# Kernel optimization log

Hardware: AMD Instinct MI355X
Metric: run time of the kernel (lower is better)

## Reference

```python
import jax, jax.numpy as jnp
import numpy as np

EMBED_DIM = 1024
NUM_HEADS = 16
HEAD_DIM = EMBED_DIM // NUM_HEADS
N, SEQ = 4, 2048


def setup_inputs() -> dict:
    key = jax.random.key(0)
    ks = jax.random.split(key, 9)
    s = 0.02
    return {
        "keys": jax.random.normal(ks[0], (N, SEQ, EMBED_DIM), jnp.float32),
        "values": jax.random.normal(ks[1], (N, SEQ, EMBED_DIM), jnp.float32),
        "queries": jax.random.normal(ks[2], (N, SEQ, EMBED_DIM), jnp.float32),
        "mask": jax.random.randint(ks[3], (N, 1, SEQ, SEQ), 0, 2, jnp.int32),
        "Wk": jax.random.normal(ks[4], (HEAD_DIM, HEAD_DIM), jnp.float32) * s,
        "Wv": jax.random.normal(ks[5], (HEAD_DIM, HEAD_DIM), jnp.float32) * s,
        "Wq": jax.random.normal(ks[6], (HEAD_DIM, HEAD_DIM), jnp.float32) * s,
        "Wo": jax.random.normal(ks[7], (EMBED_DIM, EMBED_DIM), jnp.float32) * s,
        "bo": jax.random.normal(ks[8], (EMBED_DIM,), jnp.float32) * s,
    }


def reference(keys, values, queries, mask, Wk, Wv, Wq, Wo, bo):
    n, key_len, _ = keys.shape
    value_len = values.shape[1]
    query_len = queries.shape[1]
    # Faithful to source: direct reshape (N, L, E) -> (N, H, L, D), no transpose.
    k = keys.reshape(n, NUM_HEADS, key_len, HEAD_DIM) @ Wk.T
    v = values.reshape(n, NUM_HEADS, value_len, HEAD_DIM) @ Wv.T
    q = queries.reshape(n, NUM_HEADS, query_len, HEAD_DIM) @ Wq.T
    # Scaled by sqrt(embed_dim) as in the original (not sqrt(head_dim)).
    energy = jnp.einsum('nhqd,nhkd->nhqk', q, k) / jnp.sqrt(jnp.float32(EMBED_DIM))
    energy = jnp.where(mask == 0, jnp.float32(-1e20), energy)
    attention = jax.nn.softmax(energy, axis=-1)
    att_out = jnp.einsum('nhql,nhld->nhqd', attention, v)
    att_out = att_out.reshape(n, query_len, NUM_HEADS * HEAD_DIM)
    return att_out @ Wo.T + bo
```

## Files before the change

kernel.cpp:

```cpp
#include <hip/hip_runtime.h>

#define SEQ 2048
#define HDIM 64
#define NH 16

typedef __bf16 bf16x8 __attribute__((ext_vector_type(8)));
typedef float f32x4 __attribute__((ext_vector_type(4)));
typedef unsigned short u16x8 __attribute__((ext_vector_type(8)));
typedef unsigned short u16x4 __attribute__((ext_vector_type(4)));
typedef _Float16 f16x4 __attribute__((ext_vector_type(4)));
typedef unsigned int u32x2 __attribute__((ext_vector_type(2)));
typedef unsigned long long u64;

__device__ __forceinline__ unsigned short f2bf(float f) {
  unsigned int u = __builtin_bit_cast(unsigned int, f);
  u = (u + 0x7FFFu + ((u >> 16) & 1u)) >> 16;
  return (unsigned short)u;
}

__device__ __forceinline__ bf16x8 cvt8(f32x4 a, f32x4 b) {
  u16x8 u;
  u[0] = f2bf(a[0]); u[1] = f2bf(a[1]); u[2] = f2bf(a[2]); u[3] = f2bf(a[3]);
  u[4] = f2bf(b[0]); u[5] = f2bf(b[1]); u[6] = f2bf(b[2]); u[7] = f2bf(b[3]);
  return __builtin_bit_cast(bf16x8, u);
}

__device__ __forceinline__ f32x4 mfma16(bf16x8 a, bf16x8 b, f32x4 c) {
  return __builtin_amdgcn_mfma_f32_16x16x32_bf16(a, b, c, 0, 0, 0);
}
__device__ __forceinline__ f32x4 mfma16h(f16x4 a, f16x4 b, f32x4 c) {
  return __builtin_amdgcn_mfma_f32_16x16x16f16(a, b, c, 0, 0, 0);
}

__device__ __forceinline__ f16x4 pk4h(float a, float b, float cc, float d) {
  auto h0 = __builtin_amdgcn_cvt_pkrtz(a, b);
  auto h1 = __builtin_amdgcn_cvt_pkrtz(cc, d);
  u32x2 u = { __builtin_bit_cast(unsigned int, h0),
              __builtin_bit_cast(unsigned int, h1) };
  return __builtin_bit_cast(f16x4, u);
}

#define QSCALE 0.045084220027780106f

__global__ __launch_bounds__(256) void qkv_proj(
    const float* __restrict__ keys, const float* __restrict__ values,
    const float* __restrict__ queries,
    const float* __restrict__ Wk, const float* __restrict__ Wv,
    const float* __restrict__ Wq,
    unsigned short* __restrict__ kb, unsigned short* __restrict__ vb,
    unsigned short* __restrict__ qb)
{
  const int which = blockIdx.y;
  const float* __restrict__ in = (which == 0) ? keys : (which == 1) ? values : queries;
  const float* __restrict__ W  = (which == 0) ? Wk   : (which == 1) ? Wv     : Wq;
  unsigned short* __restrict__ op = (which == 0) ? kb : (which == 1) ? vb : qb;
  const float osc = (which == 2) ? QSCALE : 1.0f;
  const bool asf16 = (which == 1);

  const int tid = threadIdx.x;
  const int w = tid >> 6, lane = tid & 63, c = lane & 15, quad = lane >> 4;

  bf16x8 bw[4][2];
  #pragma unroll
  for (int nt = 0; nt < 4; ++nt)
    #pragma unroll
    for (int hh = 0; hh < 2; ++hh) {
      const float* wr = W + (nt * 16 + c) * 64 + hh * 32 + quad * 8;
      bw[nt][hh] = cvt8(*(const f32x4*)wr, *(const f32x4*)(wr + 4));
    }

  const int m00 = blockIdx.x * 256 + w * 64;
  #pragma unroll
  for (int s = 0; s < 4; ++s) {
    const int m0 = m00 + s * 16;
    const float* xr = in + (size_t)(m0 + c) * 64;
    bf16x8 a0 = cvt8(*(const f32x4*)(xr + quad * 8), *(const f32x4*)(xr + quad * 8 + 4));
    bf16x8 a1 = cvt8(*(const f32x4*)(xr + 32 + quad * 8), *(const f32x4*)(xr + 36 + quad * 8));
    f32x4 acc[4] = {};
    #pragma unroll
    for (int nt = 0; nt < 4; ++nt) {
      acc[nt] = mfma16(a0, bw[nt][0], acc[nt]);
      acc[nt] = mfma16(a1, bw[nt][1], acc[nt]);
    }
    #pragma unroll
    for (int nt = 0; nt < 4; ++nt)
      #pragma unroll
      for (int r = 0; r < 4; ++r) {
        float v = acc[nt][r] * osc;
        unsigned short bits = asf16
            ? __builtin_bit_cast(unsigned short, (_Float16)v) : f2bf(v);
        op[(size_t)(m0 + quad * 4 + r) * 64 + nt * 16 + c] = bits;
      }
  }
}

__global__ __launch_bounds__(256) void cvt_wo(const float* __restrict__ src,
                                              unsigned short* __restrict__ dst)
{
  int i = (blockIdx.x * 256 + threadIdx.x) * 4;
  f32x4 v = *reinterpret_cast<const f32x4*>(src + i);
  u16x4 o;
  o[0] = f2bf(v[0]); o[1] = f2bf(v[1]); o[2] = f2bf(v[2]); o[3] = f2bf(v[3]);
  *reinterpret_cast<u16x4*>(dst + i) = o;
}

__global__ __launch_bounds__(256) void maskpack(const int* __restrict__ mask,
                                                u64* __restrict__ bits)
{
  const int wid = blockIdx.x * 4 + (threadIdx.x >> 6);
  const int lane = threadIdx.x & 63;
  const int* src = mask + (size_t)wid * 1024 + lane;
  u64* dst = bits + (size_t)wid * 16;
  #pragma unroll
  for (int i = 0; i < 16; ++i) {
    u64 b = __ballot(src[i * 64] != 0);
    if (lane == 0) dst[i] = b;
  }
}

__global__ __launch_bounds__(256, 4) void attn3(
    const unsigned short* __restrict__ qb, const unsigned short* __restrict__ kb,
    const unsigned short* __restrict__ vb, const u64* __restrict__ mbits,
    unsigned short* __restrict__ att)
{
  __shared__ __attribute__((aligned(16))) unsigned short Kl[64][72];
  __shared__ __attribute__((aligned(16))) unsigned short Vt[64][76];

  const int tid = threadIdx.x;
  const int w = tid >> 6, lane = tid & 63, c = lane & 15, quad = lane >> 4;
  const int h = blockIdx.y, n = blockIdx.z;
  const int q0 = blockIdx.x * 128;
  const size_t hb = (size_t)(n * NH + h) * (SEQ * HDIM);

  bf16x8 aq[2][2];
  #pragma unroll
  for (int qt = 0; qt < 2; ++qt) {
    const unsigned short* qr = qb + hb + (size_t)(q0 + qt * 64 + w * 16 + c) * HDIM;
    aq[qt][0] = *reinterpret_cast<const bf16x8*>(qr + quad * 8);
    aq[qt][1] = *reinterpret_cast<const bf16x8*>(qr + 32 + quad * 8);
  }

  f32x4 o[2][4] = {};
  f32x4 psv[2] = {};

  const u64* mb = mbits + ((size_t)n * SEQ + q0 + w * 16 + c) * 32;

  const int krow = tid >> 1, kcol = (tid & 1) * 32;
  const int vg = (tid >> 3) & 15, vd8 = tid & 7;

  for (int k0 = 0; k0 < SEQ; k0 += 64) {
    const int step = k0 >> 6;
    __syncthreads();
    if (tid < 128) {
      const unsigned short* s = kb + hb + (size_t)(k0 + krow) * HDIM + kcol;
      #pragma unroll
      for (int i = 0; i < 4; ++i)
        *(u16x8*)&Kl[krow][kcol + i * 8] = *(const u16x8*)(s + i * 8);
    } else {
      const unsigned short* s = vb + hb + (size_t)(k0 + vg * 4) * HDIM + vd8 * 8;
      u16x8 r0 = *(const u16x8*)(s);
      u16x8 r1 = *(const u16x8*)(s + HDIM);
      u16x8 r2 = *(const u16x8*)(s + 2 * HDIM);
      u16x8 r3 = *(const u16x8*)(s + 3 * HDIM);
      #pragma unroll
      for (int j = 0; j < 8; ++j) {
        u16x4 pk = { r0[j], r1[j], r2[j], r3[j] };
        *(u16x4*)&Vt[vd8 * 8 + j][vg * 4] = pk;
      }
    }
    __syncthreads();

    f32x4 e[2][4] = {};
    #pragma unroll
    for (int t = 0; t < 4; ++t) {
      bf16x8 kf0 = *reinterpret_cast<const bf16x8*>(&Kl[t * 16 + c][quad * 8]);
      bf16x8 kf1 = *reinterpret_cast<const bf16x8*>(&Kl[t * 16 + c][32 + quad * 8]);
      #pragma unroll
      for (int qt = 0; qt < 2; ++qt) {
        e[qt][t] = mfma16(kf0, aq[qt][0], e[qt][t]);
        e[qt][t] = mfma16(kf1, aq[qt][1], e[qt][t]);
      }
    }

    f16x4 pf[2][4];
    #pragma unroll
    for (int qt = 0; qt < 2; ++qt) {
      u64 bits = mb[(size_t)qt * 2048 + step] >> (quad * 4);
      unsigned int lo = (unsigned int)bits;
      unsigned int hi = (unsigned int)(bits >> 32);
      #pragma unroll
      for (int t = 0; t < 4; ++t) {
        unsigned int b = (t & 2) ? hi : lo;
        b >>= (t & 1) * 16;
        f32x4 ev = e[qt][t];
        float p0 = (b & 1u)        ? exp2f(ev[0]) : 0.0f;
        float p1 = ((b >> 1) & 1u) ? exp2f(ev[1]) : 0.0f;
        float p2 = ((b >> 2) & 1u) ? exp2f(ev[2]) : 0.0f;
        float p3 = ((b >> 3) & 1u) ? exp2f(ev[3]) : 0.0f;
        f32x4 pv = { p0, p1, p2, p3 };
        psv[qt] += pv;
        pf[qt][t] = pk4h(p0, p1, p2, p3);
      }
    }

    #pragma unroll
    for (int dt = 0; dt < 4; ++dt) {
      #pragma unroll
      for (int t = 0; t < 4; ++t) {
        f16x4 vf = __builtin_bit_cast(f16x4,
            *(const u16x4*)&Vt[dt * 16 + c][t * 16 + quad * 4]);
        o[0][dt] = mfma16h(vf, pf[0][t], o[0][dt]);
        o[1][dt] = mfma16h(vf, pf[1][t], o[1][dt]);
      }
    }
  }

  #pragma unroll
  for (int qt = 0; qt < 2; ++qt) {
    float s = (psv[qt][0] + psv[qt][1]) + (psv[qt][2] + psv[qt][3]);
    s += __shfl_xor(s, 16);
    s += __shfl_xor(s, 32);
    float inv = 1.0f / s;
    unsigned short* orow =
        att + hb + (size_t)(q0 + qt * 64 + w * 16 + c) * HDIM + quad * 4;
    #pragma unroll
    for (int dt = 0; dt < 4; ++dt) {
      u16x4 pk = { f2bf(o[qt][dt][0] * inv), f2bf(o[qt][dt][1] * inv),
                   f2bf(o[qt][dt][2] * inv), f2bf(o[qt][dt][3] * inv) };
      *(u16x4*)(orow + dt * 16) = pk;
    }
  }
}

__global__ __launch_bounds__(256) void out_proj2(
    const unsigned short* __restrict__ att, const unsigned short* __restrict__ wob,
    const float* __restrict__ bo, float* __restrict__ out)
{
  __shared__ __attribute__((aligned(16))) unsigned short As[128][72];
  __shared__ __attribute__((aligned(16))) unsigned short Bs[128][72];

  const int nb = blockIdx.x, mbk = blockIdx.y;
  const int tid = threadIdx.x;
  const int w = tid >> 6, lane = tid & 63, c = lane & 15, quad = lane >> 4;
  const int wm = w & 1, wn = w >> 1;
  const int m0 = mbk * 128, n0 = nb * 128;
  const int srow = tid >> 1, scol = (tid & 1) * 32;

  f32x4 acc[4][4] = {};

  for (int k0 = 0; k0 < 1024; k0 += 64) {
    __syncthreads();
    {
      const unsigned short* sa = att + (size_t)(m0 + srow) * 1024 + k0 + scol;
      const unsigned short* sb = wob + (size_t)(n0 + srow) * 1024 + k0 + scol;
      #pragma unroll
      for (int i = 0; i < 4; ++i)
        *(u16x8*)&As[srow][scol + i * 8] = *(const u16x8*)(sa + i * 8);
      #pragma unroll
      for (int i = 0; i < 4; ++i)
        *(u16x8*)&Bs[srow][scol + i * 8] = *(const u16x8*)(sb + i * 8);
    }
    __syncthreads();

    #pragma unroll
    for (int kk = 0; kk < 64; kk += 32) {
      bf16x8 af[4];
      #pragma unroll
      for (int mt = 0; mt < 4; ++mt)
        af[mt] = *reinterpret_cast<const bf16x8*>(&As[wm * 64 + mt * 16 + c][kk + quad * 8]);
      #pragma unroll
      for (int nt = 0; nt < 4; ++nt) {
        bf16x8 bf_ = *reinterpret_cast<const bf16x8*>(&Bs[wn * 64 + nt * 16 + c][kk + quad * 8]);
        #pragma unroll
        for (int mt = 0; mt < 4; ++mt)
          acc[mt][nt] = mfma16(af[mt], bf_, acc[mt][nt]);
      }
    }
  }

  #pragma unroll
  for (int nt = 0; nt < 4; ++nt) {
    const int col = n0 + wn * 64 + nt * 16 + c;
    const float bias = bo[col];
    #pragma unroll
    for (int mt = 0; mt < 4; ++mt)
      #pragma unroll
      for (int r = 0; r < 4; ++r)
        out[(size_t)(m0 + wm * 64 + mt * 16 + quad * 4 + r) * 1024 + col] =
            acc[mt][nt][r] + bias;
  }
}

extern "C" void kernel_launch(void* const* d_in, const int* in_sizes, int n_in,
                              void* d_out, int out_size, void* d_ws, size_t ws_size,
                              hipStream_t stream) {
  const float* keys    = (const float*)d_in[0];
  const float* values  = (const float*)d_in[1];
  const float* queries = (const float*)d_in[2];
  const int*   mask    = (const int*)d_in[3];
  const float* Wk      = (const float*)d_in[4];
  const float* Wv      = (const float*)d_in[5];
  const float* Wq      = (const float*)d_in[6];
  const float* Wo      = (const float*)d_in[7];
  const float* bo      = (const float*)d_in[8];
  float* out = (float*)d_out;

  const size_t T = (size_t)4 * NH * SEQ * HDIM;
  unsigned short* ws  = (unsigned short*)d_ws;
  unsigned short* kb  = ws;
  unsigned short* vb  = kb + T;
  unsigned short* qb  = vb + T;
  unsigned short* att = qb + T;
  unsigned short* wob = att + T;
  u64* mbits = (u64*)(wob + 1024 * 1024);

  qkv_proj<<<dim3(512, 3), 256, 0, stream>>>(keys, values, queries,
                                             Wk, Wv, Wq, kb, vb, qb);
  cvt_wo<<<dim3(1024), 256, 0, stream>>>(Wo, wob);
  maskpack<<<dim3(4096), 256, 0, stream>>>(mask, mbits);
  attn3<<<dim3(16, NH, 4), 256, 0, stream>>>(qb, kb, vb, mbits, att);
  out_proj2<<<dim3(8, 64), 256, 0, stream>>>(att, wob, bo, out);
}
```

Measured before the change: 377.8 us.

## Prefetch K/V tiles, mask via LUT, MFMA row sums, smaller out-proj tiles

Several changes land at once. The attention kernel now prefetches the next K/V tile into registers while the current one is processed, applies the mask by ANDing packed fp16 probabilities with a shared-memory lookup table, and computes softmax denominators with an extra MFMA against a ones vector instead of shuffles. qkv_proj swaps its MFMA operands so it can write packed 4-element stores. out_proj uses 64-row M tiles to double the block count. These add register pressure, and the fp16 row sums lose some precision.

```diff
diff --git a/kernel.cpp b/kernel.cpp
--- a/kernel.cpp
+++ b/kernel.cpp
@@ -60,13 +60,13 @@
   const int tid = threadIdx.x;
   const int w = tid >> 6, lane = tid & 63, c = lane & 15, quad = lane >> 4;
 
-  bf16x8 bw[4][2];
-  #pragma unroll
-  for (int nt = 0; nt < 4; ++nt)
+  bf16x8 aw[4][2];
+  #pragma unroll
+  for (int dt = 0; dt < 4; ++dt)
     #pragma unroll
     for (int hh = 0; hh < 2; ++hh) {
-      const float* wr = W + (nt * 16 + c) * 64 + hh * 32 + quad * 8;
-      bw[nt][hh] = cvt8(*(const f32x4*)wr, *(const f32x4*)(wr + 4));
+      const float* wr = W + (dt * 16 + c) * 64 + hh * 32 + quad * 8;
+      aw[dt][hh] = cvt8(*(const f32x4*)wr, *(const f32x4*)(wr + 4));
     }
 
   const int m00 = blockIdx.x * 256 + w * 64;
@@ -74,23 +74,27 @@
   for (int s = 0; s < 4; ++s) {
     const int m0 = m00 + s * 16;
     const float* xr = in + (size_t)(m0 + c) * 64;
-    bf16x8 a0 = cvt8(*(const f32x4*)(xr + quad * 8), *(const f32x4*)(xr + quad * 8 + 4));
-    bf16x8 a1 = cvt8(*(const f32x4*)(xr + 32 + quad * 8), *(const f32x4*)(xr + 36 + quad * 8));
+    bf16x8 x0 = cvt8(*(const f32x4*)(xr + quad * 8), *(const f32x4*)(xr + quad * 8 + 4));
+    bf16x8 x1 = cvt8(*(const f32x4*)(xr + 32 + quad * 8), *(const f32x4*)(xr + 36 + quad * 8));
     f32x4 acc[4] = {};
     #pragma unroll
-    for (int nt = 0; nt < 4; ++nt) {
-      acc[nt] = mfma16(a0, bw[nt][0], acc[nt]);
-      acc[nt] = mfma16(a1, bw[nt][1], acc[nt]);
-    }
-    #pragma unroll
-    for (int nt = 0; nt < 4; ++nt)
-      #pragma unroll
-      for (int r = 0; r < 4; ++r) {
-        float v = acc[nt][r] * osc;
-        unsigned short bits = asf16
-            ? __builtin_bit_cast(unsigned short, (_Float16)v) : f2bf(v);
-        op[(size_t)(m0 + quad * 4 + r) * 64 + nt * 16 + c] = bits;
-      }
+    for (int dt = 0; dt < 4; ++dt) {
+      acc[dt] = mfma16(aw[dt][0], x0, acc[dt]);
+      acc[dt] = mfma16(aw[dt][1], x1, acc[dt]);
+    }
+    unsigned short* orow = op + (size_t)(m0 + c) * 64 + quad * 4;
+    #pragma unroll
+    for (int dt = 0; dt < 4; ++dt) {
+      u16x4 pk;
+      if (asf16) {
+        pk = __builtin_bit_cast(u16x4,
+            pk4h(acc[dt][0], acc[dt][1], acc[dt][2], acc[dt][3]));
+      } else {
+        pk[0] = f2bf(acc[dt][0] * osc); pk[1] = f2bf(acc[dt][1] * osc);
+        pk[2] = f2bf(acc[dt][2] * osc); pk[3] = f2bf(acc[dt][3] * osc);
+      }
+      *(u16x4*)(orow + dt * 16) = pk;
+    }
   }
 }
 
@@ -118,13 +122,14 @@
   }
 }
 
-__global__ __launch_bounds__(256, 4) void attn3(
+__global__ __launch_bounds__(256, 4) void attn4(
     const unsigned short* __restrict__ qb, const unsigned short* __restrict__ kb,
     const unsigned short* __restrict__ vb, const u64* __restrict__ mbits,
     unsigned short* __restrict__ att)
 {
   __shared__ __attribute__((aligned(16))) unsigned short Kl[64][72];
   __shared__ __attribute__((aligned(16))) unsigned short Vt[64][76];
+  __shared__ unsigned int mlut[16][2];
 
   const int tid = threadIdx.x;
   const int w = tid >> 6, lane = tid & 63, c = lane & 15, quad = lane >> 4;
@@ -132,6 +137,12 @@
   const int q0 = blockIdx.x * 128;
   const size_t hb = (size_t)(n * NH + h) * (SEQ * HDIM);
 
+  if (tid < 16) {
+    unsigned m = tid;
+    mlut[m][0] = ((m & 1u) ? 0xFFFFu : 0u) | ((m & 2u) ? 0xFFFF0000u : 0u);
+    mlut[m][1] = ((m & 4u) ? 0xFFFFu : 0u) | ((m & 8u) ? 0xFFFF0000u : 0u);
+  }
+
   bf16x8 aq[2][2];
   #pragma unroll
   for (int qt = 0; qt < 2; ++qt) {
@@ -141,31 +152,57 @@
   }
 
   f32x4 o[2][4] = {};
-  f32x4 psv[2] = {};
+  f32x4 osum[2] = {};
+  const f16x4 ones = {(_Float16)1.f, (_Float16)1.f, (_Float16)1.f, (_Float16)1.f};
 
   const u64* mb = mbits + ((size_t)n * SEQ + q0 + w * 16 + c) * 32;
 
+  const bool isK = tid < 128;
   const int krow = tid >> 1, kcol = (tid & 1) * 32;
   const int vg = (tid >> 3) & 15, vd8 = tid & 7;
 
-  for (int k0 = 0; k0 < SEQ; k0 += 64) {
-    const int step = k0 >> 6;
+  const unsigned short* kptr = kb + hb + (size_t)krow * HDIM + kcol;
+  const unsigned short* vptr = vb + hb + (size_t)(vg * 4) * HDIM + vd8 * 8;
+
+  u16x8 st0, st1, st2, st3;
+  if (isK) {
+    st0 = *(const u16x8*)(kptr);
+    st1 = *(const u16x8*)(kptr + 8);
+    st2 = *(const u16x8*)(kptr + 16);
+    st3 = *(const u16x8*)(kptr + 24);
+  } else {
+    st0 = *(const u16x8*)(vptr);
+    st1 = *(const u16x8*)(vptr + HDIM);
+    st2 = *(const u16x8*)(vptr + 2 * HDIM);
+    st3 = *(const u16x8*)(vptr + 3 * HDIM);
+  }
+
+  for (int step = 0; step < 32; ++step) {
     __syncthreads();
-    if (tid < 128) {
-      const unsigned short* s = kb + hb + (size_t)(k0 + krow) * HDIM + kcol;
-      #pragma unroll
-      for (int i = 0; i < 4; ++i)
-        *(u16x8*)&Kl[krow][kcol + i * 8] = *(const u16x8*)(s + i * 8);
+    if (isK) {
+      *(u16x8*)&Kl[krow][kcol]      = st0;
+      *(u16x8*)&Kl[krow][kcol + 8]  = st1;
+      *(u16x8*)&Kl[krow][kcol + 16] = st2;
+      *(u16x8*)&Kl[krow][kcol + 24] = st3;
     } else {
-      const unsigned short* s = vb + hb + (size_t)(k0 + vg * 4) * HDIM + vd8 * 8;
-      u16x8 r0 = *(const u16x8*)(s);
-      u16x8 r1 = *(const u16x8*)(s + HDIM);
-      u16x8 r2 = *(const u16x8*)(s + 2 * HDIM);
-      u16x8 r3 = *(const u16x8*)(s + 3 * HDIM);
       #pragma unroll
       for (int j = 0; j < 8; ++j) {
-        u16x4 pk = { r0[j], r1[j], r2[j], r3[j] };
+        u16x4 pk = { st0[j], st1[j], st2[j], st3[j] };
         *(u16x4*)&Vt[vd8 * 8 + j][vg * 4] = pk;
+      }
+    }
+    if (step < 31) {
+      const size_t adv = (size_t)(step + 1) * 64 * HDIM;
+      if (isK) {
+        st0 = *(const u16x8*)(kptr + adv);
+        st1 = *(const u16x8*)(kptr + adv + 8);
+        st2 = *(const u16x8*)(kptr + adv + 16);
+        st3 = *(const u16x8*)(kptr + adv + 24);
+      } else {
+        st0 = *(const u16x8*)(vptr + adv);
+        st1 = *(const u16x8*)(vptr + adv + HDIM);
+        st2 = *(const u16x8*)(vptr + adv + 2 * HDIM);
+        st3 = *(const u16x8*)(vptr + adv + 3 * HDIM);
       }
     }
     __syncthreads();
@@ -182,24 +219,23 @@
       }
     }
 
+    u64 b0 = mb[step] >> (quad * 4);
+    u64 b1 = mb[2048 + step] >> (quad * 4);
+
     f16x4 pf[2][4];
     #pragma unroll
     for (int qt = 0; qt < 2; ++qt) {
-      u64 bits = mb[(size_t)qt * 2048 + step] >> (quad * 4);
-      unsigned int lo = (unsigned int)bits;
-      unsigned int hi = (unsigned int)(bits >> 32);
+      u64 bb = qt ? b1 : b0;
+      unsigned int lo = (unsigned int)bb, hi = (unsigned int)(bb >> 32);
       #pragma unroll
       for (int t = 0; t < 4; ++t) {
-        unsigned int b = (t & 2) ? hi : lo;
-        b >>= (t & 1) * 16;
+        unsigned int nib = (((t & 2) ? hi : lo) >> ((t & 1) * 16)) & 0xFu;
         f32x4 ev = e[qt][t];
-        float p0 = (b & 1u)        ? exp2f(ev[0]) : 0.0f;
-        float p1 = ((b >> 1) & 1u) ? exp2f(ev[1]) : 0.0f;
-        float p2 = ((b >> 2) & 1u) ? exp2f(ev[2]) : 0.0f;
-        float p3 = ((b >> 3) & 1u) ? exp2f(ev[3]) : 0.0f;
-        f32x4 pv = { p0, p1, p2, p3 };
-        psv[qt] += pv;
-        pf[qt][t] = pk4h(p0, p1, p2, p3);
+        f16x4 pk = pk4h(exp2f(ev[0]), exp2f(ev[1]), exp2f(ev[2]), exp2f(ev[3]));
+        u32x2 pw = __builtin_bit_cast(u32x2, pk);
+        pw[0] &= mlut[nib][0];
+        pw[1] &= mlut[nib][1];
+        pf[qt][t] = __builtin_bit_cast(f16x4, pw);
       }
     }
 
@@ -213,14 +249,16 @@
         o[1][dt] = mfma16h(vf, pf[1][t], o[1][dt]);
       }
     }
+    #pragma unroll
+    for (int t = 0; t < 4; ++t) {
+      osum[0] = mfma16h(ones, pf[0][t], osum[0]);
+      osum[1] = mfma16h(ones, pf[1][t], osum[1]);
+    }
   }
 
   #pragma unroll
   for (int qt = 0; qt < 2; ++qt) {
-    float s = (psv[qt][0] + psv[qt][1]) + (psv[qt][2] + psv[qt][3]);
-    s += __shfl_xor(s, 16);
-    s += __shfl_xor(s, 32);
-    float inv = 1.0f / s;
+    float inv = 1.0f / osum[qt][0];
     unsigned short* orow =
         att + hb + (size_t)(q0 + qt * 64 + w * 16 + c) * HDIM + quad * 4;
     #pragma unroll
@@ -232,47 +270,47 @@
   }
 }
 
-__global__ __launch_bounds__(256) void out_proj2(
+__global__ __launch_bounds__(256) void out_proj3(
     const unsigned short* __restrict__ att, const unsigned short* __restrict__ wob,
     const float* __restrict__ bo, float* __restrict__ out)
 {
-  __shared__ __attribute__((aligned(16))) unsigned short As[128][72];
+  __shared__ __attribute__((aligned(16))) unsigned short As[64][72];
   __shared__ __attribute__((aligned(16))) unsigned short Bs[128][72];
 
   const int nb = blockIdx.x, mbk = blockIdx.y;
   const int tid = threadIdx.x;
   const int w = tid >> 6, lane = tid & 63, c = lane & 15, quad = lane >> 4;
   const int wm = w & 1, wn = w >> 1;
-  const int m0 = mbk * 128, n0 = nb * 128;
-  const int srow = tid >> 1, scol = (tid & 1) * 32;
-
-  f32x4 acc[4][4] = {};
+  const int m0 = mbk * 64, n0 = nb * 128;
+  const int arow = tid >> 2, acol = (tid & 3) * 16;
+  const int brow = tid >> 1, bcol = (tid & 1) * 32;
+
+  f32x4 acc[2][4] = {};
 
   for (int k0 = 0; k0 < 1024; k0 += 64) {
     __syncthreads();
     {
-      const unsigned short* sa = att + (size_t)(m0 + srow) * 1024 + k0 + scol;
-      const unsigned short* sb = wob + (size_t)(n0 + srow) * 1024 + k0 + scol;
+      const unsigned short* sa = att + (size_t)(m0 + arow) * 1024 + k0 + acol;
+      const unsigned short* sb = wob + (size_t)(n0 + brow) * 1024 + k0 + bcol;
+      *(u16x8*)&As[arow][acol]     = *(const u16x8*)(sa);
+      *(u16x8*)&As[arow][acol + 8] = *(const u16x8*)(sa + 8);
       #pragma unroll
       for (int i = 0; i < 4; ++i)
-        *(u16x8*)&As[srow][scol + i * 8] = *(const u16x8*)(sa + i * 8);
-      #pragma unroll
-      for (int i = 0; i < 4; ++i)
-        *(u16x8*)&Bs[srow][scol + i * 8] = *(const u16x8*)(sb + i * 8);
+        *(u16x8*)&Bs[brow][bcol + i * 8] = *(const u16x8*)(sb + i * 8);
     }
     __syncthreads();
 
     #pragma unroll
     for (int kk = 0; kk < 64; kk += 32) {
-      bf16x8 af[4];
-      #pragma unroll
-      for (int mt = 0; mt < 4; ++mt)
-        af[mt] = *reinterpret_cast<const bf16x8*>(&As[wm * 64 + mt * 16 + c][kk + quad * 8]);
+      bf16x8 af[2];
+      #pragma unroll
+      for (int mt = 0; mt < 2; ++mt)
+        af[mt] = *reinterpret_cast<const bf16x8*>(&As[wm * 32 + mt * 16 + c][kk + quad * 8]);
       #pragma unroll
       for (int nt = 0; nt < 4; ++nt) {
         bf16x8 bf_ = *reinterpret_cast<const bf16x8*>(&Bs[wn * 64 + nt * 16 + c][kk + quad * 8]);
         #pragma unroll
-        for (int mt = 0; mt < 4; ++mt)
+        for (int mt = 0; mt < 2; ++mt)
           acc[mt][nt] = mfma16(af[mt], bf_, acc[mt][nt]);
       }
     }
@@ -283,10 +321,10 @@
     const int col = n0 + wn * 64 + nt * 16 + c;
     const float bias = bo[col];
     #pragma unroll
-    for (int mt = 0; mt < 4; ++mt)
+    for (int mt = 0; mt < 2; ++mt)
       #pragma unroll
       for (int r = 0; r < 4; ++r)
-        out[(size_t)(m0 + wm * 64 + mt * 16 + quad * 4 + r) * 1024 + col] =
+        out[(size_t)(m0 + wm * 32 + mt * 16 + quad * 4 + r) * 1024 + col] =
             acc[mt][nt][r] + bias;
   }
 }
@@ -318,6 +356,6 @@
                                              Wk, Wv, Wq, kb, vb, qb);
   cvt_wo<<<dim3(1024), 256, 0, stream>>>(Wo, wob);
   maskpack<<<dim3(4096), 256, 0, stream>>>(mask, mbits);
-  attn3<<<dim3(16, NH, 4), 256, 0, stream>>>(qb, kb, vb, mbits, att);
-  out_proj2<<<dim3(8, 64), 256, 0, stream>>>(att, wob, bo, out);
-}
+  attn4<<<dim3(16, NH, 4), 256, 0, stream>>>(qb, kb, vb, mbits, att);
+  out_proj3<<<dim3(8, 128), 256, 0, stream>>>(att, wob, bo, out);
+}
```

Measured after the change: 376.0 us. About the same (-0.5%).
